# Optimization experiments

Measured on AMD Instinct MI355X. Metric: run time of the kernel, lower is better.

## Reference

```python
import jax, jax.numpy as jnp
from jax import lax
import numpy as np

EPS = 1e-06


def _box_filter(x, radius):
    # Depthwise box mean with zero padding (matches F.conv2d padding=radius),
    # implemented separably: O(r) per pixel instead of O(r^2).
    C = x.shape[1]
    k = 2 * radius + 1
    dn = ('NCHW', 'OIHW', 'NCHW')
    kern_h = jnp.ones((C, 1, k, 1), x.dtype)
    kern_w = jnp.ones((C, 1, 1, k), x.dtype) / (k * k)
    y = lax.conv_general_dilated(x, kern_h, (1, 1), [(radius, radius), (0, 0)],
                                 feature_group_count=C, dimension_numbers=dn)
    return lax.conv_general_dilated(y, kern_w, (1, 1), [(0, 0), (radius, radius)],
                                    feature_group_count=C, dimension_numbers=dn)


def setup_inputs() -> dict:
    key = jax.random.key(0)
    k1, k2 = jax.random.split(key)
    I = jax.random.uniform(k1, (8, 1, 1024, 1024), dtype=jnp.float32)
    p = jax.random.uniform(k2, (8, 3, 1024, 1024), dtype=jnp.float32)
    return {"I": I, "p": p, "radius": 3}


def reference(I, p, radius):
    mean_I = _box_filter(I, radius)            # (B,1,H,W)
    mean_p = _box_filter(p, radius)            # (B,3,H,W)
    mean_Ip = _box_filter(I * p, radius)
    mean_II = _box_filter(I * I, radius)
    cov_Ip = mean_Ip - mean_I * mean_p
    var_I = mean_II - mean_I * mean_I
    a = cov_Ip / (var_I + EPS)
    b = mean_p - a * mean_I
    mean_a = _box_filter(a, radius)
    mean_b = _box_filter(b, radius)
    q = mean_a * I + mean_b
    return jnp.clip(q, 0.0, 1.0)
```

## Files before the change

kernel.cpp:

```cpp
#include <hip/hip_runtime.h>


typedef float v4 __attribute__((ext_vector_type(4)));
typedef float v2 __attribute__((ext_vector_type(2)));

#define TPB   64
#define OUTW  116
#define SEGH  64
#define HW    1024
#define NIDX  68
#define EPSF  1e-6f
#define INV49 (1.0f/49.0f)

struct St {
    v4 s14[2], s58[2];
    v4 t64[2]; v2 t62[2];
    v4 rab4[8][2]; v2 rab2[8][2];
    v4 ent[2][2];
    v4 lv[2], lvN[2];
    v2 Io, IoN;
};

template<int U>
__device__ __forceinline__ void rowStep(
    St& S, const int r, const int Yb, const int t, const int xc2,
    const bool ok0, const bool ok1, const bool sok, const int x0,
    const float* __restrict__ Ip, const float* __restrict__ P0,
    const float* __restrict__ P1, const float* __restrict__ P2,
    float* __restrict__ Q0, float* __restrict__ Q1, float* __restrict__ Q2,
    v4 (* __restrict__ c8)[2][2][NIDX],
    v4 (* __restrict__ c6A)[2][NIDX],
    v2 (* __restrict__ c6B)[2][NIDX])
{
    constexpr int SU = U & 1;
    constexpr int WS = U;
    constexpr int LS = (U + 1) & 7;

    #pragma unroll
    for (int c = 0; c < 2; ++c) {
        const v4 cE = S.ent[SU][c];
        const v4 L  = S.lv[c];
        v4 d14, d58;
        d14.x = cE.x - L.x;
        d14.y = cE.x*cE.x - L.x*L.x;
        d14.z = cE.y - L.y;
        d14.w = cE.z - L.z;
        d58.x = cE.w - L.w;
        d58.y = cE.x*cE.y - L.x*L.y;
        d58.z = cE.x*cE.z - L.x*L.z;
        d58.w = cE.x*cE.w - L.x*L.w;
        S.s14[c] += d14;
        S.s58[c] += d58;
        c8[SU][c][0][t+2] = S.s14[c];
        c8[SU][c][1][t+2] = S.s58[c];
    }
    asm volatile("" ::: "memory");

    {
        const v4 e14_1 = c8[SU][0][0][t+1], e14_2 = c8[SU][0][0][t+2],
                 e14_3 = c8[SU][0][0][t+3], e14_4 = c8[SU][0][0][t+4];
        const v4 o14_0 = c8[SU][1][0][t+0], o14_1 = c8[SU][1][0][t+1],
                 o14_2 = c8[SU][1][0][t+2], o14_3 = c8[SU][1][0][t+3];
        const v4 w14 = (e14_1 + e14_2 + e14_3) + (o14_1 + o14_2 + o14_3);
        v4 W14[2]; W14[0] = w14 + o14_0; W14[1] = w14 + e14_4;

        const v4 e58_1 = c8[SU][0][1][t+1], e58_2 = c8[SU][0][1][t+2],
                 e58_3 = c8[SU][0][1][t+3], e58_4 = c8[SU][0][1][t+4];
        const v4 o58_0 = c8[SU][1][1][t+0], o58_1 = c8[SU][1][1][t+1],
                 o58_2 = c8[SU][1][1][t+2], o58_3 = c8[SU][1][1][t+3];
        const v4 w58 = (e58_1 + e58_2 + e58_3) + (o58_1 + o58_2 + o58_3);
        v4 W58[2]; W58[0] = w58 + o58_0; W58[1] = w58 + e58_4;

        const int  yc   = Yb + r - 3;
        const bool ycok = (unsigned)yc < HW;
        const bool okc[2] = {ok0, ok1};
        #pragma unroll
        for (int c = 0; c < 2; ++c) {
            const v4 A = W14[c], B = W58[c];
            const float mi  = A.x * INV49;
            const float mii = A.y * INV49;
            const float rv  = __builtin_amdgcn_rcpf(mii - mi*mi + EPSF);
            const bool abok = ycok && okc[c];
            const float mp0 = A.z*INV49, mp1 = A.w*INV49, mp2 = B.x*INV49;
            const float a0 = (B.y*INV49 - mi*mp0)*rv;
            const float a1 = (B.z*INV49 - mi*mp1)*rv;
            const float a2 = (B.w*INV49 - mi*mp2)*rv;
            const float b0 = fmaf(-a0, mi, mp0);
            const float b1 = fmaf(-a1, mi, mp1);
            const float b2 = fmaf(-a2, mi, mp2);
            v4 ab4; ab4.x = abok?a0:0.f; ab4.y = abok?b0:0.f;
                    ab4.z = abok?a1:0.f; ab4.w = abok?b1:0.f;
            v2 ab2; ab2.x = abok?a2:0.f; ab2.y = abok?b2:0.f;
            S.t64[c] += ab4 - S.rab4[LS][c];  S.rab4[WS][c] = ab4;
            S.t62[c] += ab2 - S.rab2[LS][c];  S.rab2[WS][c] = ab2;
            c6A[SU][c][t+2] = S.t64[c];
            c6B[SU][c][t+2] = S.t62[c];
        }
    }
    asm volatile("" ::: "memory");

    {
        const int yE = Yb + r + 2;
        if ((unsigned)yE < HW) {
            const size_t ro = (size_t)yE * HW + xc2;
            const v2 vI = *(const v2*)(Ip + ro);
            const v2 va = *(const v2*)(P0 + ro);
            const v2 vb = *(const v2*)(P1 + ro);
            const v2 vc = *(const v2*)(P2 + ro);
            v4 E0, E1;
            E0.x = ok0?vI.x:0.f; E0.y = ok0?va.x:0.f; E0.z = ok0?vb.x:0.f; E0.w = ok0?vc.x:0.f;
            E1.x = ok1?vI.y:0.f; E1.y = ok1?va.y:0.f; E1.z = ok1?vb.y:0.f; E1.w = ok1?vc.y:0.f;
            S.ent[SU][0] = E0; S.ent[SU][1] = E1;
        } else {
            const v4 z = {0.f,0.f,0.f,0.f};
            S.ent[SU][0] = z; S.ent[SU][1] = z;
        }
        const int yL = Yb + r - 6;
        if (r >= 6 && (unsigned)yL < HW) {
            const size_t ro = (size_t)yL * HW + xc2;
            const v2 vI = *(const v2*)(Ip + ro);
            const v2 va = *(const v2*)(P0 + ro);
            const v2 vb = *(const v2*)(P1 + ro);
            const v2 vc = *(const v2*)(P2 + ro);
            v4 L0, L1;
            L0.x = ok0?vI.x:0.f; L0.y = ok0?va.x:0.f; L0.z = ok0?vb.x:0.f; L0.w = ok0?vc.x:0.f;
            L1.x = ok1?vI.y:0.f; L1.y = ok1?va.y:0.f; L1.z = ok1?vb.y:0.f; L1.w = ok1?vc.y:0.f;
            S.lvN[0] = L0; S.lvN[1] = L1;
        } else {
            const v4 z = {0.f,0.f,0.f,0.f};
            S.lvN[0] = z; S.lvN[1] = z;
        }
        const int yO = Yb + r - 5;
        if ((unsigned)yO < HW) {
            const size_t ro = (size_t)yO * HW + xc2;
            const v2 vio = *(const v2*)(Ip + ro);
            S.IoN.x = ok0?vio.x:0.f; S.IoN.y = ok1?vio.y:0.f;
        } else { S.IoN.x = 0.f; S.IoN.y = 0.f; }
    }

    if ((unsigned)(r - 12) <= 63u) {
        const v4 eA1 = c6A[SU][0][t+1], eA2 = c6A[SU][0][t+2],
                 eA3 = c6A[SU][0][t+3], eA4 = c6A[SU][0][t+4];
        const v4 oA0 = c6A[SU][1][t+0], oA1 = c6A[SU][1][t+1],
                 oA2 = c6A[SU][1][t+2], oA3 = c6A[SU][1][t+3];
        const v2 eB1 = c6B[SU][0][t+1], eB2 = c6B[SU][0][t+2],
                 eB3 = c6B[SU][0][t+3], eB4 = c6B[SU][0][t+4];
        const v2 oB0 = c6B[SU][1][t+0], oB1 = c6B[SU][1][t+1],
                 oB2 = c6B[SU][1][t+2], oB3 = c6B[SU][1][t+3];
        const v4 wA = (eA1+eA2+eA3) + (oA1+oA2+oA3);
        const v2 wB = (eB1+eB2+eB3) + (oB1+oB2+oB3);
        const v4 A0 = wA + oA0, A1 = wA + eA4;
        const v2 B0 = wB + oB0, B1 = wB + eB4;
        if (sok) {
            const int o = Yb + r - 6;
            const size_t ob = (size_t)o * HW + x0;
            v2 q;
            q.x = fminf(fmaxf(fmaf(A0.x*INV49, S.Io.x, A0.y*INV49), 0.f), 1.f);
            q.y = fminf(fmaxf(fmaf(A1.x*INV49, S.Io.y, A1.y*INV49), 0.f), 1.f);
            *(v2*)(Q0 + ob) = q;
            q.x = fminf(fmaxf(fmaf(A0.z*INV49, S.Io.x, A0.w*INV49), 0.f), 1.f);
            q.y = fminf(fmaxf(fmaf(A1.z*INV49, S.Io.y, A1.w*INV49), 0.f), 1.f);
            *(v2*)(Q1 + ob) = q;
            q.x = fminf(fmaxf(fmaf(B0.x*INV49, S.Io.x, B0.y*INV49), 0.f), 1.f);
            q.y = fminf(fmaxf(fmaf(B1.x*INV49, S.Io.y, B1.y*INV49), 0.f), 1.f);
            *(v2*)(Q2 + ob) = q;
        }
    }
    S.lv[0] = S.lvN[0]; S.lv[1] = S.lvN[1];
    S.Io = S.IoN;
}

__global__ __launch_bounds__(TPB, 2) void gf_kernel(
    const float* __restrict__ I, const float* __restrict__ P,
    float* __restrict__ Q)
{
    __shared__ v4 c8[2][2][2][NIDX];
    __shared__ v4 c6A[2][2][NIDX];
    __shared__ v2 c6B[2][2][NIDX];

    const int s   = blockIdx.x;
    const int seg = blockIdx.y;
    const int b   = blockIdx.z;
    const int t   = threadIdx.x;

    const int Yb = seg*SEGH - 6;
    const int x0 = s*OUTW - 6 + 2*t;
    const int x1 = x0 + 1;
    const bool ok0 = (unsigned)x0 < HW;
    const bool ok1 = (unsigned)x1 < HW;
    const int  xc2 = min(max(x0, 0), HW-2);
    const bool sok = (t >= 3) && (t <= 60) && ok0 && ok1;

    const float* Ip = I + (size_t)b*HW*HW;
    const float* P0 = P + ((size_t)b*3 + 0)*HW*HW;
    const float* P1 = P + ((size_t)b*3 + 1)*HW*HW;
    const float* P2 = P + ((size_t)b*3 + 2)*HW*HW;
    float* Q0 = Q + ((size_t)b*3 + 0)*HW*HW;
    float* Q1 = Q + ((size_t)b*3 + 1)*HW*HW;
    float* Q2 = Q + ((size_t)b*3 + 2)*HW*HW;

    {
        const v4 z4 = {0.f,0.f,0.f,0.f};
        const v2 z2 = {0.f,0.f};
        v4* a = (v4*)c8;
        #pragma unroll 2
        for (int i = t; i < 2*2*2*NIDX; i += TPB) a[i] = z4;
        v4* bb = (v4*)c6A;
        for (int i = t; i < 2*2*NIDX; i += TPB) bb[i] = z4;
        v2* cc = (v2*)c6B;
        for (int i = t; i < 2*2*NIDX; i += TPB) cc[i] = z2;
    }

    St S;
    {
        const v4 z4 = {0.f,0.f,0.f,0.f};
        const v2 z2 = {0.f,0.f};
        #pragma unroll
        for (int c = 0; c < 2; ++c) {
            S.s14[c] = z4; S.s58[c] = z4; S.t64[c] = z4; S.t62[c] = z2;
            S.lv[c] = z4; S.lvN[c] = z4;
            #pragma unroll
            for (int i = 0; i < 8; ++i) { S.rab4[i][c] = z4; S.rab2[i][c] = z2; }
        }
        S.Io = z2; S.IoN = z2;
        #pragma unroll
        for (int pr = 0; pr < 2; ++pr) {
            const int yE = Yb + pr;
            if ((unsigned)yE < HW) {
                const size_t ro = (size_t)yE * HW + xc2;
                const v2 vI = *(const v2*)(Ip + ro);
                const v2 va = *(const v2*)(P0 + ro);
                const v2 vb = *(const v2*)(P1 + ro);
                const v2 vc = *(const v2*)(P2 + ro);
                v4 E0, E1;
                E0.x = ok0?vI.x:0.f; E0.y = ok0?va.x:0.f; E0.z = ok0?vb.x:0.f; E0.w = ok0?vc.x:0.f;
                E1.x = ok1?vI.y:0.f; E1.y = ok1?va.y:0.f; E1.z = ok1?vb.y:0.f; E1.w = ok1?vc.y:0.f;
                S.ent[pr][0] = E0; S.ent[pr][1] = E1;
            } else {
                S.ent[pr][0] = z4; S.ent[pr][1] = z4;
            }
        }
    }
    __syncthreads();

    for (int m = 0; m < 9; ++m) {
        const int r0 = m*8;
        rowStep<0>(S, r0+0, Yb, t, xc2, ok0, ok1, sok, x0, Ip,P0,P1,P2, Q0,Q1,Q2, c8,c6A,c6B);
        rowStep<1>(S, r0+1, Yb, t, xc2, ok0, ok1, sok, x0, Ip,P0,P1,P2, Q0,Q1,Q2, c8,c6A,c6B);
        rowStep<2>(S, r0+2, Yb, t, xc2, ok0, ok1, sok, x0, Ip,P0,P1,P2, Q0,Q1,Q2, c8,c6A,c6B);
        rowStep<3>(S, r0+3, Yb, t, xc2, ok0, ok1, sok, x0, Ip,P0,P1,P2, Q0,Q1,Q2, c8,c6A,c6B);
        rowStep<4>(S, r0+4, Yb, t, xc2, ok0, ok1, sok, x0, Ip,P0,P1,P2, Q0,Q1,Q2, c8,c6A,c6B);
        rowStep<5>(S, r0+5, Yb, t, xc2, ok0, ok1, sok, x0, Ip,P0,P1,P2, Q0,Q1,Q2, c8,c6A,c6B);
        rowStep<6>(S, r0+6, Yb, t, xc2, ok0, ok1, sok, x0, Ip,P0,P1,P2, Q0,Q1,Q2, c8,c6A,c6B);
        rowStep<7>(S, r0+7, Yb, t, xc2, ok0, ok1, sok, x0, Ip,P0,P1,P2, Q0,Q1,Q2, c8,c6A,c6B);
    }
    rowStep<0>(S, 72, Yb, t, xc2, ok0, ok1, sok, x0, Ip,P0,P1,P2, Q0,Q1,Q2, c8,c6A,c6B);
    rowStep<1>(S, 73, Yb, t, xc2, ok0, ok1, sok, x0, Ip,P0,P1,P2, Q0,Q1,Q2, c8,c6A,c6B);
    rowStep<2>(S, 74, Yb, t, xc2, ok0, ok1, sok, x0, Ip,P0,P1,P2, Q0,Q1,Q2, c8,c6A,c6B);
    rowStep<3>(S, 75, Yb, t, xc2, ok0, ok1, sok, x0, Ip,P0,P1,P2, Q0,Q1,Q2, c8,c6A,c6B);
}

extern "C" void kernel_launch(void* const* d_in, const int* in_sizes, int n_in,
                              void* d_out, int out_size, void* d_ws, size_t ws_size,
                              hipStream_t stream) {
    const float* I = (const float*)d_in[0];
    const float* P = (const float*)d_in[1];
    float* Q = (float*)d_out;

    dim3 grid(9, 16, 8);
    gf_kernel<<<grid, TPB, 0, stream>>>(I, P, Q);
}
```

Measured before the change: 323.4 us.

## Halve segment height, cache I rows in registers, and drop redundant I loads

```diff
diff --git a/kernel.cpp b/kernel.cpp
--- a/kernel.cpp
+++ b/kernel.cpp
@@ -6,7 +6,7 @@
 
 #define TPB   64
 #define OUTW  116
-#define SEGH  64
+#define SEGH  32
 #define HW    1024
 #define NIDX  68
 #define EPSF  1e-6f
@@ -16,9 +16,9 @@
     v4 s14[2], s58[2];
     v4 t64[2]; v2 t62[2];
     v4 rab4[8][2]; v2 rab2[8][2];
+    v2 rI[8];
     v4 ent[2][2];
-    v4 lv[2], lvN[2];
-    v2 Io, IoN;
+    v2 lvp[3], lvpN[3];
 };
 
 template<int U>
@@ -32,27 +32,48 @@
     v4 (* __restrict__ c6A)[2][NIDX],
     v2 (* __restrict__ c6B)[2][NIDX])
 {
-    constexpr int SU = U & 1;
-    constexpr int WS = U;
-    constexpr int LS = (U + 1) & 7;
-
-    #pragma unroll
-    for (int c = 0; c < 2; ++c) {
-        const v4 cE = S.ent[SU][c];
-        const v4 L  = S.lv[c];
-        v4 d14, d58;
-        d14.x = cE.x - L.x;
-        d14.y = cE.x*cE.x - L.x*L.x;
-        d14.z = cE.y - L.y;
-        d14.w = cE.z - L.z;
-        d58.x = cE.w - L.w;
-        d58.y = cE.x*cE.y - L.x*L.y;
-        d58.z = cE.x*cE.z - L.x*L.z;
-        d58.w = cE.x*cE.w - L.x*L.w;
-        S.s14[c] += d14;
-        S.s58[c] += d58;
-        c8[SU][c][0][t+2] = S.s14[c];
-        c8[SU][c][1][t+2] = S.s58[c];
+    constexpr int SU  = U & 1;
+    constexpr int WS  = U;
+    constexpr int LS  = (U + 1) & 7;
+    constexpr int IOS = (U + 2) & 7;
+
+    {
+        const v4 cE0 = S.ent[SU][0], cE1 = S.ent[SU][1];
+        const v2 LI  = S.rI[LS];
+        {
+            const float Lx = LI.x;
+            const float L0 = S.lvp[0].x, L1 = S.lvp[1].x, L2 = S.lvp[2].x;
+            v4 d14, d58;
+            d14.x = cE0.x - Lx;
+            d14.y = cE0.x*cE0.x - Lx*Lx;
+            d14.z = cE0.y - L0;
+            d14.w = cE0.z - L1;
+            d58.x = cE0.w - L2;
+            d58.y = cE0.x*cE0.y - Lx*L0;
+            d58.z = cE0.x*cE0.z - Lx*L1;
+            d58.w = cE0.x*cE0.w - Lx*L2;
+            S.s14[0] += d14; S.s58[0] += d58;
+            c8[SU][0][0][t+2] = S.s14[0];
+            c8[SU][0][1][t+2] = S.s58[0];
+        }
+        {
+            const float Lx = LI.y;
+            const float L0 = S.lvp[0].y, L1 = S.lvp[1].y, L2 = S.lvp[2].y;
+            v4 d14, d58;
+            d14.x = cE1.x - Lx;
+            d14.y = cE1.x*cE1.x - Lx*Lx;
+            d14.z = cE1.y - L0;
+            d14.w = cE1.z - L1;
+            d58.x = cE1.w - L2;
+            d58.y = cE1.x*cE1.y - Lx*L0;
+            d58.z = cE1.x*cE1.z - Lx*L1;
+            d58.w = cE1.x*cE1.w - Lx*L2;
+            S.s14[1] += d14; S.s58[1] += d58;
+            c8[SU][1][0][t+2] = S.s14[1];
+            c8[SU][1][1][t+2] = S.s58[1];
+        }
+        v2 nI; nI.x = cE0.x; nI.y = cE1.x;
+        S.rI[WS] = nI;
     }
     asm volatile("" ::: "memory");
 
@@ -101,7 +122,7 @@
 
     {
         const int yE = Yb + r + 2;
-        if ((unsigned)yE < HW) {
+        if (r <= 41 && (unsigned)yE < HW) {
             const size_t ro = (size_t)yE * HW + xc2;
             const v2 vI = *(const v2*)(Ip + ro);
             const v2 va = *(const v2*)(P0 + ro);
@@ -116,29 +137,23 @@
             S.ent[SU][0] = z; S.ent[SU][1] = z;
         }
         const int yL = Yb + r - 6;
-        if (r >= 6 && (unsigned)yL < HW) {
+        if (r >= 6 && r <= 42 && (unsigned)yL < HW) {
             const size_t ro = (size_t)yL * HW + xc2;
-            const v2 vI = *(const v2*)(Ip + ro);
             const v2 va = *(const v2*)(P0 + ro);
             const v2 vb = *(const v2*)(P1 + ro);
             const v2 vc = *(const v2*)(P2 + ro);
-            v4 L0, L1;
-            L0.x = ok0?vI.x:0.f; L0.y = ok0?va.x:0.f; L0.z = ok0?vb.x:0.f; L0.w = ok0?vc.x:0.f;
-            L1.x = ok1?vI.y:0.f; L1.y = ok1?va.y:0.f; L1.z = ok1?vb.y:0.f; L1.w = ok1?vc.y:0.f;
-            S.lvN[0] = L0; S.lvN[1] = L1;
+            v2 L0, L1v, L2v;
+            L0.x  = ok0?va.x:0.f; L0.y  = ok1?va.y:0.f;
+            L1v.x = ok0?vb.x:0.f; L1v.y = ok1?vb.y:0.f;
+            L2v.x = ok0?vc.x:0.f; L2v.y = ok1?vc.y:0.f;
+            S.lvpN[0] = L0; S.lvpN[1] = L1v; S.lvpN[2] = L2v;
         } else {
-            const v4 z = {0.f,0.f,0.f,0.f};
-            S.lvN[0] = z; S.lvN[1] = z;
-        }
-        const int yO = Yb + r - 5;
-        if ((unsigned)yO < HW) {
-            const size_t ro = (size_t)yO * HW + xc2;
-            const v2 vio = *(const v2*)(Ip + ro);
-            S.IoN.x = ok0?vio.x:0.f; S.IoN.y = ok1?vio.y:0.f;
-        } else { S.IoN.x = 0.f; S.IoN.y = 0.f; }
-    }
-
-    if ((unsigned)(r - 12) <= 63u) {
+            const v2 z = {0.f,0.f};
+            S.lvpN[0] = z; S.lvpN[1] = z; S.lvpN[2] = z;
+        }
+    }
+
+    if ((unsigned)(r - 12) <= 31u) {
         const v4 eA1 = c6A[SU][0][t+1], eA2 = c6A[SU][0][t+2],
                  eA3 = c6A[SU][0][t+3], eA4 = c6A[SU][0][t+4];
         const v4 oA0 = c6A[SU][1][t+0], oA1 = c6A[SU][1][t+1],
@@ -152,22 +167,22 @@
         const v4 A0 = wA + oA0, A1 = wA + eA4;
         const v2 B0 = wB + oB0, B1 = wB + eB4;
         if (sok) {
+            const v2 io = S.rI[IOS];
             const int o = Yb + r - 6;
             const size_t ob = (size_t)o * HW + x0;
             v2 q;
-            q.x = fminf(fmaxf(fmaf(A0.x*INV49, S.Io.x, A0.y*INV49), 0.f), 1.f);
-            q.y = fminf(fmaxf(fmaf(A1.x*INV49, S.Io.y, A1.y*INV49), 0.f), 1.f);
+            q.x = fminf(fmaxf(fmaf(A0.x*INV49, io.x, A0.y*INV49), 0.f), 1.f);
+            q.y = fminf(fmaxf(fmaf(A1.x*INV49, io.y, A1.y*INV49), 0.f), 1.f);
             *(v2*)(Q0 + ob) = q;
-            q.x = fminf(fmaxf(fmaf(A0.z*INV49, S.Io.x, A0.w*INV49), 0.f), 1.f);
-            q.y = fminf(fmaxf(fmaf(A1.z*INV49, S.Io.y, A1.w*INV49), 0.f), 1.f);
+            q.x = fminf(fmaxf(fmaf(A0.z*INV49, io.x, A0.w*INV49), 0.f), 1.f);
+            q.y = fminf(fmaxf(fmaf(A1.z*INV49, io.y, A1.w*INV49), 0.f), 1.f);
             *(v2*)(Q1 + ob) = q;
-            q.x = fminf(fmaxf(fmaf(B0.x*INV49, S.Io.x, B0.y*INV49), 0.f), 1.f);
-            q.y = fminf(fmaxf(fmaf(B1.x*INV49, S.Io.y, B1.y*INV49), 0.f), 1.f);
+            q.x = fminf(fmaxf(fmaf(B0.x*INV49, io.x, B0.y*INV49), 0.f), 1.f);
+            q.y = fminf(fmaxf(fmaf(B1.x*INV49, io.y, B1.y*INV49), 0.f), 1.f);
             *(v2*)(Q2 + ob) = q;
         }
     }
-    S.lv[0] = S.lvN[0]; S.lv[1] = S.lvN[1];
-    S.Io = S.IoN;
+    S.lvp[0] = S.lvpN[0]; S.lvp[1] = S.lvpN[1]; S.lvp[2] = S.lvpN[2];
 }
 
 __global__ __launch_bounds__(TPB, 2) void gf_kernel(
@@ -203,7 +218,6 @@
         const v4 z4 = {0.f,0.f,0.f,0.f};
         const v2 z2 = {0.f,0.f};
         v4* a = (v4*)c8;
-        #pragma unroll 2
         for (int i = t; i < 2*2*2*NIDX; i += TPB) a[i] = z4;
         v4* bb = (v4*)c6A;
         for (int i = t; i < 2*2*NIDX; i += TPB) bb[i] = z4;
@@ -218,11 +232,13 @@
         #pragma unroll
         for (int c = 0; c < 2; ++c) {
             S.s14[c] = z4; S.s58[c] = z4; S.t64[c] = z4; S.t62[c] = z2;
-            S.lv[c] = z4; S.lvN[c] = z4;
             #pragma unroll
             for (int i = 0; i < 8; ++i) { S.rab4[i][c] = z4; S.rab2[i][c] = z2; }
         }
-        S.Io = z2; S.IoN = z2;
+        #pragma unroll
+        for (int i = 0; i < 8; ++i) S.rI[i] = z2;
+        S.lvp[0] = z2; S.lvp[1] = z2; S.lvp[2] = z2;
+        S.lvpN[0] = z2; S.lvpN[1] = z2; S.lvpN[2] = z2;
         #pragma unroll
         for (int pr = 0; pr < 2; ++pr) {
             const int yE = Yb + pr;
@@ -243,7 +259,7 @@
     }
     __syncthreads();
 
-    for (int m = 0; m < 9; ++m) {
+    for (int m = 0; m < 5; ++m) {
         const int r0 = m*8;
         rowStep<0>(S, r0+0, Yb, t, xc2, ok0, ok1, sok, x0, Ip,P0,P1,P2, Q0,Q1,Q2, c8,c6A,c6B);
         rowStep<1>(S, r0+1, Yb, t, xc2, ok0, ok1, sok, x0, Ip,P0,P1,P2, Q0,Q1,Q2, c8,c6A,c6B);
@@ -254,10 +270,10 @@
         rowStep<6>(S, r0+6, Yb, t, xc2, ok0, ok1, sok, x0, Ip,P0,P1,P2, Q0,Q1,Q2, c8,c6A,c6B);
         rowStep<7>(S, r0+7, Yb, t, xc2, ok0, ok1, sok, x0, Ip,P0,P1,P2, Q0,Q1,Q2, c8,c6A,c6B);
     }
-    rowStep<0>(S, 72, Yb, t, xc2, ok0, ok1, sok, x0, Ip,P0,P1,P2, Q0,Q1,Q2, c8,c6A,c6B);
-    rowStep<1>(S, 73, Yb, t, xc2, ok0, ok1, sok, x0, Ip,P0,P1,P2, Q0,Q1,Q2, c8,c6A,c6B);
-    rowStep<2>(S, 74, Yb, t, xc2, ok0, ok1, sok, x0, Ip,P0,P1,P2, Q0,Q1,Q2, c8,c6A,c6B);
-    rowStep<3>(S, 75, Yb, t, xc2, ok0, ok1, sok, x0, Ip,P0,P1,P2, Q0,Q1,Q2, c8,c6A,c6B);
+    rowStep<0>(S, 40, Yb, t, xc2, ok0, ok1, sok, x0, Ip,P0,P1,P2, Q0,Q1,Q2, c8,c6A,c6B);
+    rowStep<1>(S, 41, Yb, t, xc2, ok0, ok1, sok, x0, Ip,P0,P1,P2, Q0,Q1,Q2, c8,c6A,c6B);
+    rowStep<2>(S, 42, Yb, t, xc2, ok0, ok1, sok, x0, Ip,P0,P1,P2, Q0,Q1,Q2, c8,c6A,c6B);
+    rowStep<3>(S, 43, Yb, t, xc2, ok0, ok1, sok, x0, Ip,P0,P1,P2, Q0,Q1,Q2, c8,c6A,c6B);
 }
 
 extern "C" void kernel_launch(void* const* d_in, const int* in_sizes, int n_in,
@@ -267,6 +283,6 @@
     const float* P = (const float*)d_in[1];
     float* Q = (float*)d_out;
 
-    dim3 grid(9, 16, 8);
+    dim3 grid(9, 32, 8);
     gf_kernel<<<grid, TPB, 0, stream>>>(I, P, Q);
 }
```

Result: faster. 309.1 us (-4.4%).

## Switch to one column per thread with smaller tiles and more blocks

Applied to the files above, without the earlier changes.

```diff
diff --git a/kernel.cpp b/kernel.cpp
--- a/kernel.cpp
+++ b/kernel.cpp
@@ -5,178 +5,137 @@
 typedef float v2 __attribute__((ext_vector_type(2)));
 
 #define TPB   64
-#define OUTW  116
-#define SEGH  64
+#define OUTW  52
+#define SEGH  32
 #define HW    1024
-#define NIDX  68
+#define NIDX  70
 #define EPSF  1e-6f
 #define INV49 (1.0f/49.0f)
 
 struct St {
-    v4 s14[2], s58[2];
-    v4 t64[2]; v2 t62[2];
-    v4 rab4[8][2]; v2 rab2[8][2];
-    v4 ent[2][2];
-    v4 lv[2], lvN[2];
-    v2 Io, IoN;
+    v4 s14, s58;
+    v4 t64; v2 t62;
+    v4 rab4[8]; v2 rab2[8];
+    float rI[8];
+    v4 ent[2];
+    float lvp0, lvp1, lvp2;
+    float lvn0, lvn1, lvn2;
 };
 
 template<int U>
 __device__ __forceinline__ void rowStep(
-    St& S, const int r, const int Yb, const int t, const int xc2,
-    const bool ok0, const bool ok1, const bool sok, const int x0,
+    St& S, const int r, const int Yb, const int t, const int xc,
+    const bool ok, const bool sok, const int x,
     const float* __restrict__ Ip, const float* __restrict__ P0,
     const float* __restrict__ P1, const float* __restrict__ P2,
     float* __restrict__ Q0, float* __restrict__ Q1, float* __restrict__ Q2,
-    v4 (* __restrict__ c8)[2][2][NIDX],
-    v4 (* __restrict__ c6A)[2][NIDX],
-    v2 (* __restrict__ c6B)[2][NIDX])
+    v4* __restrict__ c8A, v4* __restrict__ c8B,
+    v4* __restrict__ c6A, v2* __restrict__ c6B)
 {
-    constexpr int SU = U & 1;
-    constexpr int WS = U;
-    constexpr int LS = (U + 1) & 7;
-
-    #pragma unroll
-    for (int c = 0; c < 2; ++c) {
-        const v4 cE = S.ent[SU][c];
-        const v4 L  = S.lv[c];
+    constexpr int WS  = U;
+    constexpr int LS  = (U + 1) & 7;
+    constexpr int IOS = (U + 2) & 7;
+
+    {
+        const v4 E = S.ent[U & 1];
+        const float LI = S.rI[LS];
         v4 d14, d58;
-        d14.x = cE.x - L.x;
-        d14.y = cE.x*cE.x - L.x*L.x;
-        d14.z = cE.y - L.y;
-        d14.w = cE.z - L.z;
-        d58.x = cE.w - L.w;
-        d58.y = cE.x*cE.y - L.x*L.y;
-        d58.z = cE.x*cE.z - L.x*L.z;
-        d58.w = cE.x*cE.w - L.x*L.w;
-        S.s14[c] += d14;
-        S.s58[c] += d58;
-        c8[SU][c][0][t+2] = S.s14[c];
-        c8[SU][c][1][t+2] = S.s58[c];
+        d14.x = E.x - LI;
+        d14.y = E.x*E.x - LI*LI;
+        d14.z = E.y - S.lvp0;
+        d14.w = E.z - S.lvp1;
+        d58.x = E.w - S.lvp2;
+        d58.y = E.x*E.y - LI*S.lvp0;
+        d58.z = E.x*E.z - LI*S.lvp1;
+        d58.w = E.x*E.w - LI*S.lvp2;
+        S.s14 += d14; S.s58 += d58;
+        c8A[t+3] = S.s14;
+        c8B[t+3] = S.s58;
+        S.rI[WS] = E.x;
     }
     asm volatile("" ::: "memory");
 
-    {
-        const v4 e14_1 = c8[SU][0][0][t+1], e14_2 = c8[SU][0][0][t+2],
-                 e14_3 = c8[SU][0][0][t+3], e14_4 = c8[SU][0][0][t+4];
-        const v4 o14_0 = c8[SU][1][0][t+0], o14_1 = c8[SU][1][0][t+1],
-                 o14_2 = c8[SU][1][0][t+2], o14_3 = c8[SU][1][0][t+3];
-        const v4 w14 = (e14_1 + e14_2 + e14_3) + (o14_1 + o14_2 + o14_3);
-        v4 W14[2]; W14[0] = w14 + o14_0; W14[1] = w14 + e14_4;
-
-        const v4 e58_1 = c8[SU][0][1][t+1], e58_2 = c8[SU][0][1][t+2],
-                 e58_3 = c8[SU][0][1][t+3], e58_4 = c8[SU][0][1][t+4];
-        const v4 o58_0 = c8[SU][1][1][t+0], o58_1 = c8[SU][1][1][t+1],
-                 o58_2 = c8[SU][1][1][t+2], o58_3 = c8[SU][1][1][t+3];
-        const v4 w58 = (e58_1 + e58_2 + e58_3) + (o58_1 + o58_2 + o58_3);
-        v4 W58[2]; W58[0] = w58 + o58_0; W58[1] = w58 + e58_4;
-
+    if (r >= 5) {
+        const v4 A = ((c8A[t+0] + c8A[t+1]) + (c8A[t+2] + c8A[t+3]))
+                   + ((c8A[t+4] + c8A[t+5]) + c8A[t+6]);
+        const v4 B = ((c8B[t+0] + c8B[t+1]) + (c8B[t+2] + c8B[t+3]))
+                   + ((c8B[t+4] + c8B[t+5]) + c8B[t+6]);
         const int  yc   = Yb + r - 3;
-        const bool ycok = (unsigned)yc < HW;
-        const bool okc[2] = {ok0, ok1};
-        #pragma unroll
-        for (int c = 0; c < 2; ++c) {
-            const v4 A = W14[c], B = W58[c];
-            const float mi  = A.x * INV49;
-            const float mii = A.y * INV49;
-            const float rv  = __builtin_amdgcn_rcpf(mii - mi*mi + EPSF);
-            const bool abok = ycok && okc[c];
-            const float mp0 = A.z*INV49, mp1 = A.w*INV49, mp2 = B.x*INV49;
-            const float a0 = (B.y*INV49 - mi*mp0)*rv;
-            const float a1 = (B.z*INV49 - mi*mp1)*rv;
-            const float a2 = (B.w*INV49 - mi*mp2)*rv;
-            const float b0 = fmaf(-a0, mi, mp0);
-            const float b1 = fmaf(-a1, mi, mp1);
-            const float b2 = fmaf(-a2, mi, mp2);
-            v4 ab4; ab4.x = abok?a0:0.f; ab4.y = abok?b0:0.f;
-                    ab4.z = abok?a1:0.f; ab4.w = abok?b1:0.f;
-            v2 ab2; ab2.x = abok?a2:0.f; ab2.y = abok?b2:0.f;
-            S.t64[c] += ab4 - S.rab4[LS][c];  S.rab4[WS][c] = ab4;
-            S.t62[c] += ab2 - S.rab2[LS][c];  S.rab2[WS][c] = ab2;
-            c6A[SU][c][t+2] = S.t64[c];
-            c6B[SU][c][t+2] = S.t62[c];
-        }
+        const bool abok = ok && ((unsigned)yc < HW);
+        const float mi  = A.x * INV49;
+        const float mii = A.y * INV49;
+        const float rv  = __builtin_amdgcn_rcpf(mii - mi*mi + EPSF);
+        const float mp0 = A.z*INV49, mp1 = A.w*INV49, mp2 = B.x*INV49;
+        const float a0 = (B.y*INV49 - mi*mp0)*rv;
+        const float a1 = (B.z*INV49 - mi*mp1)*rv;
+        const float a2 = (B.w*INV49 - mi*mp2)*rv;
+        const float b0 = fmaf(-a0, mi, mp0);
+        const float b1 = fmaf(-a1, mi, mp1);
+        const float b2 = fmaf(-a2, mi, mp2);
+        v4 ab4; v2 ab2;
+        ab4.x = abok?a0:0.f; ab4.y = abok?b0:0.f;
+        ab4.z = abok?a1:0.f; ab4.w = abok?b1:0.f;
+        ab2.x = abok?a2:0.f; ab2.y = abok?b2:0.f;
+        S.t64 += ab4 - S.rab4[LS];  S.rab4[WS] = ab4;
+        S.t62 += ab2 - S.rab2[LS];  S.rab2[WS] = ab2;
+        c6A[t+3] = S.t64;
+        c6B[t+3] = S.t62;
     }
     asm volatile("" ::: "memory");
 
-    {
+    if (r <= 41) {
         const int yE = Yb + r + 2;
         if ((unsigned)yE < HW) {
-            const size_t ro = (size_t)yE * HW + xc2;
-            const v2 vI = *(const v2*)(Ip + ro);
-            const v2 va = *(const v2*)(P0 + ro);
-            const v2 vb = *(const v2*)(P1 + ro);
-            const v2 vc = *(const v2*)(P2 + ro);
-            v4 E0, E1;
-            E0.x = ok0?vI.x:0.f; E0.y = ok0?va.x:0.f; E0.z = ok0?vb.x:0.f; E0.w = ok0?vc.x:0.f;
-            E1.x = ok1?vI.y:0.f; E1.y = ok1?va.y:0.f; E1.z = ok1?vb.y:0.f; E1.w = ok1?vc.y:0.f;
-            S.ent[SU][0] = E0; S.ent[SU][1] = E1;
+            const size_t ro = (size_t)yE*HW + xc;
+            const float vI = Ip[ro], va = P0[ro], vb = P1[ro], vc = P2[ro];
+            v4 E;
+            E.x = ok?vI:0.f; E.y = ok?va:0.f; E.z = ok?vb:0.f; E.w = ok?vc:0.f;
+            S.ent[U & 1] = E;
         } else {
             const v4 z = {0.f,0.f,0.f,0.f};
-            S.ent[SU][0] = z; S.ent[SU][1] = z;
-        }
+            S.ent[U & 1] = z;
+        }
+    }
+    if (r <= 42) {
         const int yL = Yb + r - 6;
-        if (r >= 6 && (unsigned)yL < HW) {
-            const size_t ro = (size_t)yL * HW + xc2;
-            const v2 vI = *(const v2*)(Ip + ro);
-            const v2 va = *(const v2*)(P0 + ro);
-            const v2 vb = *(const v2*)(P1 + ro);
-            const v2 vc = *(const v2*)(P2 + ro);
-            v4 L0, L1;
-            L0.x = ok0?vI.x:0.f; L0.y = ok0?va.x:0.f; L0.z = ok0?vb.x:0.f; L0.w = ok0?vc.x:0.f;
-            L1.x = ok1?vI.y:0.f; L1.y = ok1?va.y:0.f; L1.z = ok1?vb.y:0.f; L1.w = ok1?vc.y:0.f;
-            S.lvN[0] = L0; S.lvN[1] = L1;
+        if (r + 1 >= 7 && (unsigned)yL < HW) {
+            const size_t ro = (size_t)yL*HW + xc;
+            const float va = P0[ro], vb = P1[ro], vc = P2[ro];
+            S.lvn0 = ok?va:0.f; S.lvn1 = ok?vb:0.f; S.lvn2 = ok?vc:0.f;
         } else {
-            const v4 z = {0.f,0.f,0.f,0.f};
-            S.lvN[0] = z; S.lvN[1] = z;
-        }
-        const int yO = Yb + r - 5;
-        if ((unsigned)yO < HW) {
-            const size_t ro = (size_t)yO * HW + xc2;
-            const v2 vio = *(const v2*)(Ip + ro);
-            S.IoN.x = ok0?vio.x:0.f; S.IoN.y = ok1?vio.y:0.f;
-        } else { S.IoN.x = 0.f; S.IoN.y = 0.f; }
-    }
-
-    if ((unsigned)(r - 12) <= 63u) {
-        const v4 eA1 = c6A[SU][0][t+1], eA2 = c6A[SU][0][t+2],
-                 eA3 = c6A[SU][0][t+3], eA4 = c6A[SU][0][t+4];
-        const v4 oA0 = c6A[SU][1][t+0], oA1 = c6A[SU][1][t+1],
-                 oA2 = c6A[SU][1][t+2], oA3 = c6A[SU][1][t+3];
-        const v2 eB1 = c6B[SU][0][t+1], eB2 = c6B[SU][0][t+2],
-                 eB3 = c6B[SU][0][t+3], eB4 = c6B[SU][0][t+4];
-        const v2 oB0 = c6B[SU][1][t+0], oB1 = c6B[SU][1][t+1],
-                 oB2 = c6B[SU][1][t+2], oB3 = c6B[SU][1][t+3];
-        const v4 wA = (eA1+eA2+eA3) + (oA1+oA2+oA3);
-        const v2 wB = (eB1+eB2+eB3) + (oB1+oB2+oB3);
-        const v4 A0 = wA + oA0, A1 = wA + eA4;
-        const v2 B0 = wB + oB0, B1 = wB + eB4;
+            S.lvn0 = 0.f; S.lvn1 = 0.f; S.lvn2 = 0.f;
+        }
+    }
+
+    if (r >= 12) {
+        const v4 A6 = ((c6A[t+0] + c6A[t+1]) + (c6A[t+2] + c6A[t+3]))
+                    + ((c6A[t+4] + c6A[t+5]) + c6A[t+6]);
+        const v2 B6 = ((c6B[t+0] + c6B[t+1]) + (c6B[t+2] + c6B[t+3]))
+                    + ((c6B[t+4] + c6B[t+5]) + c6B[t+6]);
         if (sok) {
+            const float io = S.rI[IOS];
             const int o = Yb + r - 6;
-            const size_t ob = (size_t)o * HW + x0;
-            v2 q;
-            q.x = fminf(fmaxf(fmaf(A0.x*INV49, S.Io.x, A0.y*INV49), 0.f), 1.f);
-            q.y = fminf(fmaxf(fmaf(A1.x*INV49, S.Io.y, A1.y*INV49), 0.f), 1.f);
-            *(v2*)(Q0 + ob) = q;
-            q.x = fminf(fmaxf(fmaf(A0.z*INV49, S.Io.x, A0.w*INV49), 0.f), 1.f);
-            q.y = fminf(fmaxf(fmaf(A1.z*INV49, S.Io.y, A1.w*INV49), 0.f), 1.f);
-            *(v2*)(Q1 + ob) = q;
-            q.x = fminf(fmaxf(fmaf(B0.x*INV49, S.Io.x, B0.y*INV49), 0.f), 1.f);
-            q.y = fminf(fmaxf(fmaf(B1.x*INV49, S.Io.y, B1.y*INV49), 0.f), 1.f);
-            *(v2*)(Q2 + ob) = q;
-        }
-    }
-    S.lv[0] = S.lvN[0]; S.lv[1] = S.lvN[1];
-    S.Io = S.IoN;
+            const size_t ob = (size_t)o * HW + x;
+            float q;
+            q = fminf(fmaxf(fmaf(A6.x*INV49, io, A6.y*INV49), 0.f), 1.f);
+            Q0[ob] = q;
+            q = fminf(fmaxf(fmaf(A6.z*INV49, io, A6.w*INV49), 0.f), 1.f);
+            Q1[ob] = q;
+            q = fminf(fmaxf(fmaf(B6.x*INV49, io, B6.y*INV49), 0.f), 1.f);
+            Q2[ob] = q;
+        }
+    }
+    S.lvp0 = S.lvn0; S.lvp1 = S.lvn1; S.lvp2 = S.lvn2;
 }
 
-__global__ __launch_bounds__(TPB, 2) void gf_kernel(
+__global__ __launch_bounds__(TPB, 4) void gf_kernel(
     const float* __restrict__ I, const float* __restrict__ P,
     float* __restrict__ Q)
 {
-    __shared__ v4 c8[2][2][2][NIDX];
-    __shared__ v4 c6A[2][2][NIDX];
-    __shared__ v2 c6B[2][2][NIDX];
+    __shared__ v4 c8A[NIDX];
+    __shared__ v4 c8B[NIDX];
+    __shared__ v4 c6A[NIDX];
+    __shared__ v2 c6B[NIDX];
 
     const int s   = blockIdx.x;
     const int seg = blockIdx.y;
@@ -184,12 +143,10 @@
     const int t   = threadIdx.x;
 
     const int Yb = seg*SEGH - 6;
-    const int x0 = s*OUTW - 6 + 2*t;
-    const int x1 = x0 + 1;
-    const bool ok0 = (unsigned)x0 < HW;
-    const bool ok1 = (unsigned)x1 < HW;
-    const int  xc2 = min(max(x0, 0), HW-2);
-    const bool sok = (t >= 3) && (t <= 60) && ok0 && ok1;
+    const int x  = s*OUTW - 6 + t;
+    const bool ok = (unsigned)x < HW;
+    const int  xc = min(max(x, 0), HW-1);
+    const bool sok = (t >= 6) && (t <= 57) && ok;
 
     const float* Ip = I + (size_t)b*HW*HW;
     const float* P0 = P + ((size_t)b*3 + 0)*HW*HW;
@@ -202,62 +159,52 @@
     {
         const v4 z4 = {0.f,0.f,0.f,0.f};
         const v2 z2 = {0.f,0.f};
-        v4* a = (v4*)c8;
-        #pragma unroll 2
-        for (int i = t; i < 2*2*2*NIDX; i += TPB) a[i] = z4;
-        v4* bb = (v4*)c6A;
-        for (int i = t; i < 2*2*NIDX; i += TPB) bb[i] = z4;
-        v2* cc = (v2*)c6B;
-        for (int i = t; i < 2*2*NIDX; i += TPB) cc[i] = z2;
+        for (int i = t; i < NIDX; i += TPB) {
+            c8A[i] = z4; c8B[i] = z4; c6A[i] = z4; c6B[i] = z2;
+        }
     }
 
     St S;
     {
         const v4 z4 = {0.f,0.f,0.f,0.f};
         const v2 z2 = {0.f,0.f};
+        S.s14 = z4; S.s58 = z4; S.t64 = z4; S.t62 = z2;
         #pragma unroll
-        for (int c = 0; c < 2; ++c) {
-            S.s14[c] = z4; S.s58[c] = z4; S.t64[c] = z4; S.t62[c] = z2;
-            S.lv[c] = z4; S.lvN[c] = z4;
-            #pragma unroll
-            for (int i = 0; i < 8; ++i) { S.rab4[i][c] = z4; S.rab2[i][c] = z2; }
-        }
-        S.Io = z2; S.IoN = z2;
+        for (int i = 0; i < 8; ++i) {
+            S.rab4[i] = z4; S.rab2[i] = z2; S.rI[i] = 0.f;
+        }
+        S.lvp0=S.lvp1=S.lvp2=0.f; S.lvn0=S.lvn1=S.lvn2=0.f;
         #pragma unroll
-        for (int pr = 0; pr < 2; ++pr) {
-            const int yE = Yb + pr;
+        for (int q = 0; q < 2; ++q) {
+            const int yE = Yb + q;
             if ((unsigned)yE < HW) {
-                const size_t ro = (size_t)yE * HW + xc2;
-                const v2 vI = *(const v2*)(Ip + ro);
-                const v2 va = *(const v2*)(P0 + ro);
-                const v2 vb = *(const v2*)(P1 + ro);
-                const v2 vc = *(const v2*)(P2 + ro);
-                v4 E0, E1;
-                E0.x = ok0?vI.x:0.f; E0.y = ok0?va.x:0.f; E0.z = ok0?vb.x:0.f; E0.w = ok0?vc.x:0.f;
-                E1.x = ok1?vI.y:0.f; E1.y = ok1?va.y:0.f; E1.z = ok1?vb.y:0.f; E1.w = ok1?vc.y:0.f;
-                S.ent[pr][0] = E0; S.ent[pr][1] = E1;
+                const size_t ro = (size_t)yE*HW + xc;
+                const float vI = Ip[ro], va = P0[ro], vb = P1[ro], vc = P2[ro];
+                v4 E;
+                E.x = ok?vI:0.f; E.y = ok?va:0.f; E.z = ok?vb:0.f; E.w = ok?vc:0.f;
+                S.ent[q] = E;
             } else {
-                S.ent[pr][0] = z4; S.ent[pr][1] = z4;
+                S.ent[q] = z4;
             }
         }
     }
     __syncthreads();
 
-    for (int m = 0; m < 9; ++m) {
+    for (int m = 0; m < 5; ++m) {
         const int r0 = m*8;
-        rowStep<0>(S, r0+0, Yb, t, xc2, ok0, ok1, sok, x0, Ip,P0,P1,P2, Q0,Q1,Q2, c8,c6A,c6B);
-        rowStep<1>(S, r0+1, Yb, t, xc2, ok0, ok1, sok, x0, Ip,P0,P1,P2, Q0,Q1,Q2, c8,c6A,c6B);
-        rowStep<2>(S, r0+2, Yb, t, xc2, ok0, ok1, sok, x0, Ip,P0,P1,P2, Q0,Q1,Q2, c8,c6A,c6B);
-        rowStep<3>(S, r0+3, Yb, t, xc2, ok0, ok1, sok, x0, Ip,P0,P1,P2, Q0,Q1,Q2, c8,c6A,c6B);
-        rowStep<4>(S, r0+4, Yb, t, xc2, ok0, ok1, sok, x0, Ip,P0,P1,P2, Q0,Q1,Q2, c8,c6A,c6B);
-        rowStep<5>(S, r0+5, Yb, t, xc2, ok0, ok1, sok, x0, Ip,P0,P1,P2, Q0,Q1,Q2, c8,c6A,c6B);
-        rowStep<6>(S, r0+6, Yb, t, xc2, ok0, ok1, sok, x0, Ip,P0,P1,P2, Q0,Q1,Q2, c8,c6A,c6B);
-        rowStep<7>(S, r0+7, Yb, t, xc2, ok0, ok1, sok, x0, Ip,P0,P1,P2, Q0,Q1,Q2, c8,c6A,c6B);
-    }
-    rowStep<0>(S, 72, Yb, t, xc2, ok0, ok1, sok, x0, Ip,P0,P1,P2, Q0,Q1,Q2, c8,c6A,c6B);
-    rowStep<1>(S, 73, Yb, t, xc2, ok0, ok1, sok, x0, Ip,P0,P1,P2, Q0,Q1,Q2, c8,c6A,c6B);
-    rowStep<2>(S, 74, Yb, t, xc2, ok0, ok1, sok, x0, Ip,P0,P1,P2, Q0,Q1,Q2, c8,c6A,c6B);
-    rowStep<3>(S, 75, Yb, t, xc2, ok0, ok1, sok, x0, Ip,P0,P1,P2, Q0,Q1,Q2, c8,c6A,c6B);
+        rowStep<0>(S, r0+0, Yb, t, xc, ok, sok, x, Ip,P0,P1,P2, Q0,Q1,Q2, c8A,c8B,c6A,c6B);
+        rowStep<1>(S, r0+1, Yb, t, xc, ok, sok, x, Ip,P0,P1,P2, Q0,Q1,Q2, c8A,c8B,c6A,c6B);
+        rowStep<2>(S, r0+2, Yb, t, xc, ok, sok, x, Ip,P0,P1,P2, Q0,Q1,Q2, c8A,c8B,c6A,c6B);
+        rowStep<3>(S, r0+3, Yb, t, xc, ok, sok, x, Ip,P0,P1,P2, Q0,Q1,Q2, c8A,c8B,c6A,c6B);
+        rowStep<4>(S, r0+4, Yb, t, xc, ok, sok, x, Ip,P0,P1,P2, Q0,Q1,Q2, c8A,c8B,c6A,c6B);
+        rowStep<5>(S, r0+5, Yb, t, xc, ok, sok, x, Ip,P0,P1,P2, Q0,Q1,Q2, c8A,c8B,c6A,c6B);
+        rowStep<6>(S, r0+6, Yb, t, xc, ok, sok, x, Ip,P0,P1,P2, Q0,Q1,Q2, c8A,c8B,c6A,c6B);
+        rowStep<7>(S, r0+7, Yb, t, xc, ok, sok, x, Ip,P0,P1,P2, Q0,Q1,Q2, c8A,c8B,c6A,c6B);
+    }
+    rowStep<0>(S, 40, Yb, t, xc, ok, sok, x, Ip,P0,P1,P2, Q0,Q1,Q2, c8A,c8B,c6A,c6B);
+    rowStep<1>(S, 41, Yb, t, xc, ok, sok, x, Ip,P0,P1,P2, Q0,Q1,Q2, c8A,c8B,c6A,c6B);
+    rowStep<2>(S, 42, Yb, t, xc, ok, sok, x, Ip,P0,P1,P2, Q0,Q1,Q2, c8A,c8B,c6A,c6B);
+    rowStep<3>(S, 43, Yb, t, xc, ok, sok, x, Ip,P0,P1,P2, Q0,Q1,Q2, c8A,c8B,c6A,c6B);
 }
 
 extern "C" void kernel_launch(void* const* d_in, const int* in_sizes, int n_in,
@@ -267,6 +214,6 @@
     const float* P = (const float*)d_in[1];
     float* Q = (float*)d_out;
 
-    dim3 grid(9, 16, 8);
+    dim3 grid(20, 32, 8);
     gf_kernel<<<grid, TPB, 0, stream>>>(I, P, Q);
 }
```

Result: slower. 350.2 us (+8.3%).
